# Kernel optimization log

Hardware: AMD Instinct MI355X
Metric: run time of the kernel (lower is better)

Reference implementation:

```python
import jax, jax.numpy as jnp
import numpy as np

B, T, D = 1, 2048, 4096
N, K, H = 32, 8, 128
SLOTS = 32768
THETA = 500000.0
NEG_INF = -1e30


def apply_rope(x, positions, theta=THETA):
    # x: [B, heads, T, H]; positions: [T] int32. Llama half-split rotary.
    h = x.shape[-1]
    inv_freq = 1.0 / (theta ** (jnp.arange(0, h, 2, dtype=jnp.float32) / h))  # [H/2]
    ang = positions.astype(jnp.float32)[:, None] * inv_freq[None, :]          # [T, H/2]
    cos, sin = jnp.cos(ang), jnp.sin(ang)
    x1, x2 = x[..., : h // 2], x[..., h // 2 :]
    return jnp.concatenate([x1 * cos - x2 * sin, x2 * cos + x1 * sin], axis=-1).astype(x.dtype)


def setup_inputs() -> dict:
    key = jax.random.key(0)
    ks = jax.random.split(key, 5)
    x = jax.random.normal(ks[0], (B, T, D), jnp.float32)
    wq = jax.random.normal(ks[1], (N, D, H), jnp.float32) * (D ** -0.5)
    wk = jax.random.normal(ks[2], (K, D, H), jnp.float32) * (D ** -0.5)
    wv = jax.random.normal(ks[3], (K, D, H), jnp.float32) * (D ** -0.5)
    wo = jax.random.normal(ks[4], (N, H, D), jnp.float32) * ((N * H) ** -0.5)
    k_cache = jnp.zeros((SLOTS, K, H), jnp.float32)
    v_cache = jnp.zeros((SLOTS, K, H), jnp.float32)
    positions = jnp.arange(T, dtype=jnp.int32)
    write_indices = jnp.arange(T, dtype=jnp.int32)  # paged-cache slot per token, in [0, SLOTS)
    return dict(x=x, wq=wq, wk=wk, wv=wv, wo=wo, k_cache=k_cache, v_cache=v_cache,
                positions=positions, write_indices=write_indices)


def reference(x, wq, wk, wv, wo, k_cache, v_cache, positions, write_indices):
    # QKV projections (per-head einsum, as in the module)
    q = jnp.einsum('btd,ndh->bnth', x, wq)            # [B,N,T,H]
    k = jnp.einsum('btd,kdh->bkth', x, wk)            # [B,K,T,H]
    v = jnp.einsum('btd,kdh->bkth', x, wv)            # [B,K,T,H]
    # RoPE on q and k, then q scaling by head_dim**-0.5 (applied to q as in source)
    q = apply_rope(q, positions) * (H ** -0.5)
    k = apply_rope(k, positions)
    # KV-cache scatter write (B=1): cache layout [slot, kv_head, head_dim]
    k_cache = k_cache.at[write_indices].set(jnp.transpose(k[0], (1, 0, 2)))
    v_cache = v_cache.at[write_indices].set(jnp.transpose(v[0], (1, 0, 2)))
    # Prefill causal GQA attention over the current sequence
    g = N // K
    qg = q.reshape(B, K, g, T, H)
    scores = jnp.einsum('bkgth,bksh->bkgts', qg, k)   # [B,K,G,T,T]
    mask = positions[:, None] >= positions[None, :]   # causal
    scores = jnp.where(mask, scores, NEG_INF)
    p = jax.nn.softmax(scores, axis=-1)
    attn = jnp.einsum('bkgts,bksh->bkgth', p, v).reshape(B, N, T, H)
    o = jnp.einsum('bnth,nhd->btd', attn, wo)         # [B,T,D]
    return k_cache, v_cache, o
```

## Files before the change

kernel.cpp:

```cpp
#include <hip/hip_runtime.h>
#include <stdint.h>

#define T_SEQ   2048
#define D_MODEL 4096
#define NQ      32
#define NKV     8
#define HD      128
#define NSLOTS  32768
#define L2THETA_64 0.29580575976911624f
#define QSCALE_LOG2E 0.12751743126f

typedef __bf16 bf16;
typedef bf16  bf16x8 __attribute__((ext_vector_type(8)));
typedef float f32x4  __attribute__((ext_vector_type(4)));

#define AS1 __attribute__((address_space(1)))
#define AS3 __attribute__((address_space(3)))

__device__ __forceinline__ void async_ld16(const bf16* g, bf16* l) {
  __builtin_amdgcn_global_load_lds((AS1 void*)(uintptr_t)g, (AS3 void*)l, 16, 0, 0);
}

__global__ __launch_bounds__(256) void convert_bf16(const float* __restrict__ src,
                                                    bf16* __restrict__ dst, int n8) {
  int i = blockIdx.x * blockDim.x + threadIdx.x;
  if (i >= n8) return;
  const float4* s = (const float4*)src + (size_t)i * 2;
  float4 a = s[0], b = s[1];
  bf16x8 o;
  o[0]=(bf16)a.x; o[1]=(bf16)a.y; o[2]=(bf16)a.z; o[3]=(bf16)a.w;
  o[4]=(bf16)b.x; o[5]=(bf16)b.y; o[6]=(bf16)b.z; o[7]=(bf16)b.w;
  *((bf16x8*)dst + i) = o;
}

__global__ __launch_bounds__(256) void transpose_w(const float* __restrict__ src,
                                                   bf16* __restrict__ dst,
                                                   int rows, int cols) {
  __shared__ float tile[32][33];
  const int z = blockIdx.z;
  src += (size_t)z * rows * cols;
  dst += (size_t)z * rows * cols;
  const int c0 = blockIdx.x * 32;
  const int r0 = blockIdx.y * 32;
  const int tx = threadIdx.x;
  const int ty = threadIdx.y;
#pragma unroll
  for (int j = 0; j < 32; j += 8)
    tile[ty + j][tx] = src[(size_t)(r0 + ty + j) * cols + c0 + tx];
  __syncthreads();
#pragma unroll
  for (int j = 0; j < 32; j += 8)
    dst[(size_t)(c0 + ty + j) * rows + r0 + tx] = (bf16)tile[tx][ty + j];
}

__global__ __launch_bounds__(256) void transpose_v(const bf16* __restrict__ src,
                                                   bf16* __restrict__ dst) {
  __shared__ bf16 tile[32][33];
  const int z  = blockIdx.z;
  const int h0 = blockIdx.x * 32;
  const int t0 = blockIdx.y * 32;
  const int tx = threadIdx.x;
  const int ty = threadIdx.y;
  const bf16* s = src + (size_t)z * T_SEQ * HD;
  bf16* d       = dst + (size_t)z * T_SEQ * HD;
#pragma unroll
  for (int j = 0; j < 32; j += 8)
    tile[ty + j][tx] = s[(size_t)(t0 + ty + j) * HD + h0 + tx];
  __syncthreads();
#pragma unroll
  for (int j = 0; j < 32; j += 8)
    d[(size_t)(h0 + ty + j) * T_SEQ + t0 + tx] = tile[tx][ty + j];
}

__global__ __launch_bounds__(256) void mark_slots(const int* __restrict__ wind,
                                                  uint32_t* __restrict__ bm) {
  const int tid = threadIdx.x;
  for (int i = tid; i < NSLOTS / 32; i += 256) bm[i] = 0u;
  __syncthreads();
  for (int i = tid; i < T_SEQ; i += 256) {
    const int s = wind[i];
    atomicOr(&bm[s >> 5], 1u << (s & 31));
  }
}

__global__ __launch_bounds__(256) void gemm_bt(
    const bf16* __restrict__ A, const bf16* __restrict__ Bt, int Kd, int mode,
    bf16* __restrict__ qb, bf16* __restrict__ kb, bf16* __restrict__ vb,
    float* __restrict__ kc_out, float* __restrict__ vc_out,
    const int* __restrict__ positions, const int* __restrict__ wind,
    float* __restrict__ o_out,
    const float* __restrict__ kc_src, const float* __restrict__ vc_src,
    const uint32_t* __restrict__ slotmap) {
  const int tid  = threadIdx.x;

  if (mode == 1 && blockIdx.y >= (D_MODEL / 128)) {
    const int cb   = (blockIdx.y - D_MODEL / 128) * gridDim.x + blockIdx.x;
    const int nblk = 16 * gridDim.x;
    for (int s = cb; s < NSLOTS; s += nblk) {
      if (slotmap[s >> 5] & (1u << (s & 31))) continue;
      const size_t base = (size_t)s * (NKV * HD);
      f32x4 kv = __builtin_nontemporal_load((const f32x4*)(kc_src + base) + tid);
      f32x4 vv = __builtin_nontemporal_load((const f32x4*)(vc_src + base) + tid);
      __builtin_nontemporal_store(kv, (f32x4*)(kc_out + base) + tid);
      __builtin_nontemporal_store(vv, (f32x4*)(vc_out + base) + tid);
    }
    return;
  }

  __shared__ bf16 As[128 * 32];
  __shared__ bf16 Bs[128 * 32];
  const int wid  = tid >> 6;
  const int lane = tid & 63;
  const int quad = lane >> 4;
  const int l15  = lane & 15;
  const int m0 = blockIdx.x * 128;
  const int n0 = blockIdx.y * 128;

  const int srow = tid >> 2;
  const int scol = (tid & 3) * 8;
  const bf16* Ag0 = A  + (size_t)(m0 + srow) * Kd + scol;
  const bf16* Ag1 = Ag0 + (size_t)64 * Kd;
  const bf16* Bg0 = Bt + (size_t)(n0 + srow) * Kd + scol;
  const bf16* Bg1 = Bg0 + (size_t)64 * Kd;
  bf16* Al0 = As + tid * 8;
  bf16* Al1 = As + (tid + 256) * 8;
  bf16* Bl0 = Bs + tid * 8;
  bf16* Bl1 = Bs + (tid + 256) * 8;

  const f32x4 fz = {0.f, 0.f, 0.f, 0.f};
  f32x4 acc[2][8];
#pragma unroll
  for (int mi = 0; mi < 2; ++mi)
#pragma unroll
    for (int ni = 0; ni < 8; ++ni) acc[mi][ni] = fz;

  const int mrow = wid * 32;
  for (int k0 = 0; k0 < Kd; k0 += 32) {
    async_ld16(Ag0 + k0, Al0);
    async_ld16(Ag1 + k0, Al1);
    async_ld16(Bg0 + k0, Bl0);
    async_ld16(Bg1 + k0, Bl1);
    __syncthreads();
    bf16x8 af[2], bfr[8];
#pragma unroll
    for (int mi = 0; mi < 2; ++mi)
      af[mi] = *(const bf16x8*)(As + (mrow + mi * 16 + l15) * 32 + quad * 8);
#pragma unroll
    for (int ni = 0; ni < 8; ++ni)
      bfr[ni] = *(const bf16x8*)(Bs + (ni * 16 + l15) * 32 + quad * 8);
#pragma unroll
    for (int mi = 0; mi < 2; ++mi)
#pragma unroll
      for (int ni = 0; ni < 8; ++ni)
        acc[mi][ni] = __builtin_amdgcn_mfma_f32_16x16x32_bf16(af[mi], bfr[ni], acc[mi][ni], 0, 0, 0);
    __syncthreads();
  }

  if (mode == 1) {
#pragma unroll
    for (int mi = 0; mi < 2; ++mi)
#pragma unroll
      for (int ni = 0; ni < 8; ++ni)
#pragma unroll
        for (int r = 0; r < 4; ++r) {
          int trow = m0 + mrow + mi * 16 + quad * 4 + r;
          o_out[(size_t)trow * D_MODEL + n0 + ni * 16 + l15] = acc[mi][ni][r];
        }
  } else {
    const int head = blockIdx.y;
#pragma unroll
    for (int mi = 0; mi < 2; ++mi) {
#pragma unroll
      for (int r = 0; r < 4; ++r) {
        const int trow = m0 + mrow + mi * 16 + quad * 4 + r;
        const float pos = (float)positions[trow];
        const int slot = (head >= 32) ? wind[trow] : 0;
#pragma unroll
        for (int ni = 0; ni < 4; ++ni) {
          const int h1 = ni * 16 + l15;
          float a1 = acc[mi][ni][r];
          float a2 = acc[mi][ni + 4][r];
          float o1, o2;
          if (head < 40) {
            float ang = pos * exp2f((float)h1 * -L2THETA_64);
            float sn, cs;
            sincosf(ang, &sn, &cs);
            o1 = a1 * cs - a2 * sn;
            o2 = a2 * cs + a1 * sn;
          } else { o1 = a1; o2 = a2; }
          if (head < 32) {
            o1 *= QSCALE_LOG2E; o2 *= QSCALE_LOG2E;
            bf16* qp = qb + ((size_t)head * T_SEQ + trow) * HD + h1;
            qp[0]  = (bf16)o1;
            qp[64] = (bf16)o2;
          } else if (head < 40) {
            const int kvh = head - 32;
            bf16* kp = kb + ((size_t)kvh * T_SEQ + trow) * HD + h1;
            kp[0]  = (bf16)o1;
            kp[64] = (bf16)o2;
            float* cp = kc_out + ((size_t)slot * NKV + kvh) * HD + h1;
            cp[0]  = o1;
            cp[64] = o2;
          } else {
            const int kvh = head - 40;
            bf16* vp = vb + ((size_t)kvh * T_SEQ + trow) * HD + h1;
            vp[0]  = (bf16)o1;
            vp[64] = (bf16)o2;
            float* cp = vc_out + ((size_t)slot * NKV + kvh) * HD + h1;
            cp[0]  = o1;
            cp[64] = o2;
          }
        }
      }
    }
  }
}

__global__ __launch_bounds__(256, 2) void attn_fused(
    const bf16* __restrict__ qb, const bf16* __restrict__ kb,
    const bf16* __restrict__ vt, bf16* __restrict__ attnb) {
  __shared__ bf16 Ks [64 * 128];
  __shared__ bf16 Vts[128 * 64];
  __shared__ bf16 Ps [4 * 32 * 72];
  const int tid  = threadIdx.x;
  const int wid  = tid >> 6;
  const int lane = tid & 63;
  const int quad = lane >> 4;
  const int l15  = lane & 15;
  const int head = blockIdx.y;
  const int kv   = head >> 2;
  int bt = blockIdx.x;
  if (head & 16) bt = (T_SEQ / 128 - 1) - bt;
  const int t0b  = bt * 128;
  const int t0w  = t0b + wid * 32;

  bf16x8 qf[2][4];
#pragma unroll
  for (int mi = 0; mi < 2; ++mi) {
    const bf16* qp = qb + ((size_t)head * T_SEQ + t0w + mi * 16 + l15) * HD + quad * 8;
#pragma unroll
    for (int ck = 0; ck < 4; ++ck) qf[mi][ck] = *(const bf16x8*)(qp + ck * 32);
  }

  const f32x4 fz = {0.f, 0.f, 0.f, 0.f};
  f32x4 oacc[2][8];
#pragma unroll
  for (int mi = 0; mi < 2; ++mi)
#pragma unroll
    for (int ch = 0; ch < 8; ++ch) oacc[mi][ch] = fz;
  float l_acc[8];
#pragma unroll
  for (int i = 0; i < 8; ++i) l_acc[i] = 0.f;

  const bf16* kbase = kb + (size_t)kv * T_SEQ * HD;
  const bf16* vbase = vt + (size_t)kv * HD * T_SEQ;
  bf16* Pw = Ps + wid * (32 * 72);

  const int nkt = 2 * bt + 2;
  for (int kt = 0; kt < nkt; ++kt) {
    const int tk0 = kt * 64;
#pragma unroll
    for (int i = 0; i < 4; ++i) {
      const int g = i * 256 + tid;
      const int k = g >> 4, c = g & 15;
      uint4 val = *(const uint4*)(kbase + (size_t)(tk0 + k) * HD + c * 8);
      *(uint4*)(Ks + k * 128 + ((c ^ (k & 15)) * 8)) = val;
    }
#pragma unroll
    for (int i = 0; i < 4; ++i) {
      const int g = i * 256 + tid;
      const int h = g >> 3, c = g & 7;
      uint4 val = *(const uint4*)(vbase + (size_t)h * T_SEQ + tk0 + c * 8);
      *(uint4*)(Vts + h * 64 + ((c ^ (h & 7)) * 8)) = val;
    }
    __syncthreads();

    f32x4 s[2][4];
#pragma unroll
    for (int mi = 0; mi < 2; ++mi)
#pragma unroll
      for (int n = 0; n < 4; ++n) s[mi][n] = fz;
#pragma unroll
    for (int n = 0; n < 4; ++n) {
      const int krow = n * 16 + l15;
#pragma unroll
      for (int ck = 0; ck < 4; ++ck) {
        const int cc = (ck * 4 + quad) ^ (krow & 15);
        bf16x8 kf = *(const bf16x8*)(Ks + krow * 128 + cc * 8);
#pragma unroll
        for (int mi = 0; mi < 2; ++mi)
          s[mi][n] = __builtin_amdgcn_mfma_f32_16x16x32_bf16(qf[mi][ck], kf, s[mi][n], 0, 0, 0);
      }
    }

    const bool domask = (tk0 + 63) > t0w;
#pragma unroll
    for (int mi = 0; mi < 2; ++mi)
#pragma unroll
      for (int r = 0; r < 4; ++r) {
        const int row = t0w + mi * 16 + quad * 4 + r;
#pragma unroll
        for (int n = 0; n < 4; ++n) {
          float p = __builtin_amdgcn_exp2f(s[mi][n][r]);
          if (domask && (tk0 + n * 16 + l15 > row)) p = 0.f;
          l_acc[mi * 4 + r] += p;
          Pw[(mi * 16 + quad * 4 + r) * 72 + n * 16 + l15] = (bf16)p;
        }
      }
    asm volatile("s_waitcnt lgkmcnt(0)" ::: "memory");

#pragma unroll
    for (int kk = 0; kk < 2; ++kk) {
      bf16x8 pf[2];
#pragma unroll
      for (int mi = 0; mi < 2; ++mi)
        pf[mi] = *(const bf16x8*)(Pw + (mi * 16 + l15) * 72 + kk * 32 + quad * 8);
#pragma unroll
      for (int ch = 0; ch < 8; ++ch) {
        const int h = ch * 16 + l15;
        const int cc = (kk * 4 + quad) ^ (h & 7);
        bf16x8 vf = *(const bf16x8*)(Vts + h * 64 + cc * 8);
#pragma unroll
        for (int mi = 0; mi < 2; ++mi)
          oacc[mi][ch] = __builtin_amdgcn_mfma_f32_16x16x32_bf16(pf[mi], vf, oacc[mi][ch], 0, 0, 0);
      }
    }
    __syncthreads();
  }

#pragma unroll
  for (int i = 0; i < 8; ++i) {
    float v = l_acc[i];
#pragma unroll
    for (int off = 1; off < 16; off <<= 1) v += __shfl_xor(v, off);
    l_acc[i] = 1.0f / v;
  }
#pragma unroll
  for (int mi = 0; mi < 2; ++mi)
#pragma unroll
    for (int r = 0; r < 4; ++r) {
      const int trow = t0w + mi * 16 + quad * 4 + r;
      const float inv = l_acc[mi * 4 + r];
#pragma unroll
      for (int ch = 0; ch < 8; ++ch)
        attnb[(size_t)trow * D_MODEL + head * HD + ch * 16 + l15] =
            (bf16)(oacc[mi][ch][r] * inv);
    }
}

extern "C" void kernel_launch(void* const* d_in, const int* in_sizes, int n_in,
                              void* d_out, int out_size, void* d_ws, size_t ws_size,
                              hipStream_t stream) {
  (void)in_sizes; (void)n_in; (void)out_size; (void)ws_size;
  const float* x     = (const float*)d_in[0];
  const float* wq    = (const float*)d_in[1];
  const float* wk    = (const float*)d_in[2];
  const float* wv    = (const float*)d_in[3];
  const float* wo    = (const float*)d_in[4];
  const float* kc_in = (const float*)d_in[5];
  const float* vc_in = (const float*)d_in[6];
  const int* positions = (const int*)d_in[7];
  const int* wind      = (const int*)d_in[8];

  float* out    = (float*)d_out;
  float* kc_out = out;
  float* vc_out = out + (size_t)NSLOTS * NKV * HD;
  float* o_out  = out + (size_t)2 * NSLOTS * NKV * HD;

  char* ws = (char*)d_ws;
  bf16* xb     = (bf16*)(ws);
  bf16* wqkv_t = (bf16*)(ws + (16ull  << 20));
  bf16* wo_t   = (bf16*)(ws + (64ull  << 20));
  bf16* qb     = (bf16*)(ws + (96ull  << 20));
  bf16* kb     = (bf16*)(ws + (112ull << 20));
  bf16* vb     = (bf16*)(ws + (116ull << 20));
  bf16* attnb  = xb;
  bf16* vt     = wqkv_t;
  uint32_t* slotmap = (uint32_t*)(ws + (24ull << 20));

  convert_bf16<<<dim3((T_SEQ * D_MODEL / 8 + 255) / 256), dim3(256), 0, stream>>>(
      x, xb, T_SEQ * D_MODEL / 8);
  transpose_w<<<dim3(HD / 32, D_MODEL / 32, NQ),  dim3(32, 8), 0, stream>>>(wq, wqkv_t, D_MODEL, HD);
  transpose_w<<<dim3(HD / 32, D_MODEL / 32, NKV), dim3(32, 8), 0, stream>>>(
      wk, wqkv_t + (size_t)32 * HD * D_MODEL, D_MODEL, HD);
  transpose_w<<<dim3(HD / 32, D_MODEL / 32, NKV), dim3(32, 8), 0, stream>>>(
      wv, wqkv_t + (size_t)40 * HD * D_MODEL, D_MODEL, HD);
  transpose_w<<<dim3(D_MODEL / 32, (NQ * HD) / 32, 1), dim3(32, 8), 0, stream>>>(
      wo, wo_t, NQ * HD, D_MODEL);

  gemm_bt<<<dim3(T_SEQ / 128, 48), dim3(256), 0, stream>>>(
      xb, wqkv_t, D_MODEL, 0, qb, kb, vb, kc_out, vc_out, positions, wind, nullptr,
      nullptr, nullptr, nullptr);
  mark_slots<<<dim3(1), dim3(256), 0, stream>>>(wind, slotmap);
  transpose_v<<<dim3(HD / 32, T_SEQ / 32, NKV), dim3(32, 8), 0, stream>>>(vb, vt);
  attn_fused<<<dim3(T_SEQ / 128, NQ), dim3(256), 0, stream>>>(qb, kb, vt, attnb);
  gemm_bt<<<dim3(T_SEQ / 128, D_MODEL / 128 + 16), dim3(256), 0, stream>>>(
      attnb, wo_t, D_MODEL, 1, nullptr, nullptr, nullptr, kc_out, vc_out,
      nullptr, nullptr, o_out, kc_in, vc_in, slotmap);
}
```

Baseline: 954.6 us.

## Double-buffer GEMM LDS tiles with async prefetch two stages ahead

The bf16 GEMM gets two LDS buffers for each operand. Global-to-LDS async loads for k-tile i+2 are issued while tile i is computed, with vmcnt waits and raw barriers replacing the old single-buffer load/sync loop, so memory latency can overlap the MFMA work. The mode argument becomes a template parameter so each instantiation drops dead branches, and setprio raises wave priority around the MFMA block. LDS use doubles, which may lower occupancy, and correctness now depends on the hand-placed vmcnt counts.

```diff
diff --git a/kernel.cpp b/kernel.cpp
--- a/kernel.cpp
+++ b/kernel.cpp
@@ -83,8 +83,9 @@
   }
 }
 
+template <int MODE>
 __global__ __launch_bounds__(256) void gemm_bt(
-    const bf16* __restrict__ A, const bf16* __restrict__ Bt, int Kd, int mode,
+    const bf16* __restrict__ A, const bf16* __restrict__ Bt, int Kd,
     bf16* __restrict__ qb, bf16* __restrict__ kb, bf16* __restrict__ vb,
     float* __restrict__ kc_out, float* __restrict__ vc_out,
     const int* __restrict__ positions, const int* __restrict__ wind,
@@ -93,7 +94,7 @@
     const uint32_t* __restrict__ slotmap) {
   const int tid  = threadIdx.x;
 
-  if (mode == 1 && blockIdx.y >= (D_MODEL / 128)) {
+  if (MODE == 1 && blockIdx.y >= (D_MODEL / 128)) {
     const int cb   = (blockIdx.y - D_MODEL / 128) * gridDim.x + blockIdx.x;
     const int nblk = 16 * gridDim.x;
     for (int s = cb; s < NSLOTS; s += nblk) {
@@ -107,8 +108,8 @@
     return;
   }
 
-  __shared__ bf16 As[128 * 32];
-  __shared__ bf16 Bs[128 * 32];
+  __shared__ bf16 As[2][128 * 32];
+  __shared__ bf16 Bs[2][128 * 32];
   const int wid  = tid >> 6;
   const int lane = tid & 63;
   const int quad = lane >> 4;
@@ -122,10 +123,6 @@
   const bf16* Ag1 = Ag0 + (size_t)64 * Kd;
   const bf16* Bg0 = Bt + (size_t)(n0 + srow) * Kd + scol;
   const bf16* Bg1 = Bg0 + (size_t)64 * Kd;
-  bf16* Al0 = As + tid * 8;
-  bf16* Al1 = As + (tid + 256) * 8;
-  bf16* Bl0 = Bs + tid * 8;
-  bf16* Bl1 = Bs + (tid + 256) * 8;
 
   const f32x4 fz = {0.f, 0.f, 0.f, 0.f};
   f32x4 acc[2][8];
@@ -135,28 +132,54 @@
     for (int ni = 0; ni < 8; ++ni) acc[mi][ni] = fz;
 
   const int mrow = wid * 32;
-  for (int k0 = 0; k0 < Kd; k0 += 32) {
-    async_ld16(Ag0 + k0, Al0);
-    async_ld16(Ag1 + k0, Al1);
-    async_ld16(Bg0 + k0, Bl0);
-    async_ld16(Bg1 + k0, Bl1);
-    __syncthreads();
+  const int nkt = Kd >> 5;
+
+  async_ld16(Ag0,      &As[0][tid * 8]);
+  async_ld16(Ag1,      &As[0][(tid + 256) * 8]);
+  async_ld16(Bg0,      &Bs[0][tid * 8]);
+  async_ld16(Bg1,      &Bs[0][(tid + 256) * 8]);
+  async_ld16(Ag0 + 32, &As[1][tid * 8]);
+  async_ld16(Ag1 + 32, &As[1][(tid + 256) * 8]);
+  async_ld16(Bg0 + 32, &Bs[1][tid * 8]);
+  async_ld16(Bg1 + 32, &Bs[1][(tid + 256) * 8]);
+
+  for (int i = 0; i < nkt; ++i) {
+    const bf16* Asc = As[i & 1];
+    const bf16* Bsc = Bs[i & 1];
+    if (i + 1 < nkt) asm volatile("s_waitcnt vmcnt(4)" ::: "memory");
+    else             asm volatile("s_waitcnt vmcnt(0)" ::: "memory");
+    __builtin_amdgcn_s_barrier();
+
     bf16x8 af[2], bfr[8];
 #pragma unroll
     for (int mi = 0; mi < 2; ++mi)
-      af[mi] = *(const bf16x8*)(As + (mrow + mi * 16 + l15) * 32 + quad * 8);
+      af[mi] = *(const bf16x8*)(Asc + (mrow + mi * 16 + l15) * 32 + quad * 8);
 #pragma unroll
     for (int ni = 0; ni < 8; ++ni)
-      bfr[ni] = *(const bf16x8*)(Bs + (ni * 16 + l15) * 32 + quad * 8);
+      bfr[ni] = *(const bf16x8*)(Bsc + (ni * 16 + l15) * 32 + quad * 8);
+
+    __builtin_amdgcn_s_setprio(1);
 #pragma unroll
     for (int mi = 0; mi < 2; ++mi)
 #pragma unroll
       for (int ni = 0; ni < 8; ++ni)
         acc[mi][ni] = __builtin_amdgcn_mfma_f32_16x16x32_bf16(af[mi], bfr[ni], acc[mi][ni], 0, 0, 0);
-    __syncthreads();
-  }
-
-  if (mode == 1) {
+    __builtin_amdgcn_s_setprio(0);
+
+    asm volatile("" ::: "memory");
+    __builtin_amdgcn_s_barrier();
+    if (i + 2 < nkt) {
+      const int k0 = (i + 2) * 32;
+      bf16* Ad = (bf16*)As[i & 1];
+      bf16* Bd = (bf16*)Bs[i & 1];
+      async_ld16(Ag0 + k0, Ad + tid * 8);
+      async_ld16(Ag1 + k0, Ad + (tid + 256) * 8);
+      async_ld16(Bg0 + k0, Bd + tid * 8);
+      async_ld16(Bg1 + k0, Bd + (tid + 256) * 8);
+    }
+  }
+
+  if (MODE == 1) {
 #pragma unroll
     for (int mi = 0; mi < 2; ++mi)
 #pragma unroll
@@ -388,13 +411,13 @@
   transpose_w<<<dim3(D_MODEL / 32, (NQ * HD) / 32, 1), dim3(32, 8), 0, stream>>>(
       wo, wo_t, NQ * HD, D_MODEL);
 
-  gemm_bt<<<dim3(T_SEQ / 128, 48), dim3(256), 0, stream>>>(
-      xb, wqkv_t, D_MODEL, 0, qb, kb, vb, kc_out, vc_out, positions, wind, nullptr,
+  gemm_bt<0><<<dim3(T_SEQ / 128, 48), dim3(256), 0, stream>>>(
+      xb, wqkv_t, D_MODEL, qb, kb, vb, kc_out, vc_out, positions, wind, nullptr,
       nullptr, nullptr, nullptr);
   mark_slots<<<dim3(1), dim3(256), 0, stream>>>(wind, slotmap);
   transpose_v<<<dim3(HD / 32, T_SEQ / 32, NKV), dim3(32, 8), 0, stream>>>(vb, vt);
   attn_fused<<<dim3(T_SEQ / 128, NQ), dim3(256), 0, stream>>>(qb, kb, vt, attnb);
-  gemm_bt<<<dim3(T_SEQ / 128, D_MODEL / 128 + 16), dim3(256), 0, stream>>>(
-      attnb, wo_t, D_MODEL, 1, nullptr, nullptr, nullptr, kc_out, vc_out,
+  gemm_bt<1><<<dim3(T_SEQ / 128, D_MODEL / 128 + 16), dim3(256), 0, stream>>>(
+      attnb, wo_t, D_MODEL, nullptr, nullptr, nullptr, kc_out, vc_out,
       nullptr, nullptr, o_out, kc_in, vc_in, slotmap);
 }
```

Result: faster. 912.0 us (-4.5%).
